# Kernel optimization log

Hardware: AMD Instinct MI355X
Metric: run time of the kernel (lower is better)

The kernel has to match this reference:

```python
import jax, jax.numpy as jnp
import numpy as np

EPS = 1e-12  # matches torch F.normalize default eps

def _l2_normalize(x):
    # torch.nn.functional.normalize: x / max(||x||_2, eps)
    n = jnp.sqrt(jnp.sum(x * x, axis=-1, keepdims=True))
    return x / jnp.maximum(n, EPS)

def setup_inputs() -> dict:
    key = jax.random.key(0)
    kq, kk, kv = jax.random.split(key, 3)
    B, N, M, C = 8, 4096, 4096, 256
    return {
        "query": jax.random.normal(kq, (B, N, C), dtype=jnp.float32),
        "key": jax.random.normal(kk, (B, M, C), dtype=jnp.float32),
        "value": jax.random.normal(kv, (B, M, C), dtype=jnp.float32),
    }

def reference(query, key, value):
    B, N, C = query.shape
    q = _l2_normalize(query)          # (B, N, C)
    k = _l2_normalize(key)            # (B, M, C)
    kv = jnp.einsum('bmc,bmd->bcd', k, value)   # (B, C, C)
    context = jnp.einsum('bnc,bcd->bnd', q, kv) # (B, N, C)
    return context / N
```

## Files before the change

### kernel.cpp

```cpp
#include <hip/hip_runtime.h>

typedef __attribute__((ext_vector_type(4))) float v4f;
typedef __attribute__((ext_vector_type(8))) short short8;
typedef unsigned short u16;
typedef __attribute__((ext_vector_type(4))) unsigned short u16x4;
typedef __attribute__((ext_vector_type(8))) unsigned short u16x8;

#define CDIM 256
#define NB 8
#define NN 4096
#define MM 4096

static __device__ __forceinline__ u16 f2bf(float f) {
  unsigned u = __float_as_uint(f);
  u = (u + 0x7fffu + ((u >> 16) & 1u)) >> 16;
  return (u16)u;
}
static __device__ __forceinline__ float bf2f(u16 h) {
  return __uint_as_float(((unsigned)h) << 16);
}

__global__ __launch_bounds__(256) void knorm_kernel(const float* __restrict__ key,
                                                    float* __restrict__ sk) {
  int t = threadIdx.x;
  int lane = t & 63;
  int r = blockIdx.x * 4 + (t >> 6);
  const v4f x = *(const v4f*)(key + (size_t)r * CDIM + lane * 4);
  float ss = x[0]*x[0] + x[1]*x[1] + x[2]*x[2] + x[3]*x[3];
  #pragma unroll
  for (int m = 1; m < 64; m <<= 1) ss += __shfl_xor(ss, m);
  if (lane == 0) sk[r] = 1.0f / fmaxf(sqrtf(ss), 1e-12f);
}

__global__ __launch_bounds__(512, 2) void kv_kernel(const float* __restrict__ key,
                                                    const float* __restrict__ value,
                                                    const float* __restrict__ sk,
                                                    u16* __restrict__ partial, int KC) {
  __shared__ __align__(16) u16 knT[256 * 64];
  __shared__ __align__(16) u16 vT[256 * 64];
  int t = threadIdx.x;
  int b = blockIdx.y, s = blockIdx.x;
  int w = t >> 6, lane = t & 63, lo = lane & 15, hi = lane >> 4;
  int cstage = t & 255, wq = t >> 8;

  v4f acc[2][16];
  #pragma unroll
  for (int i = 0; i < 2; i++)
    #pragma unroll
    for (int d = 0; d < 16; d++) acc[i][d] = (v4f){0.f, 0.f, 0.f, 0.f};

  int nsc = KC >> 6;
  for (int sc = 0; sc < nsc; ++sc) {
    int mbase = s * KC + sc * 64;
    #pragma unroll
    for (int it = 0; it < 8; ++it) {
      int ml0 = it * 8 + wq * 4;
      int gr = b * MM + mbase + ml0;
      size_t grow = (size_t)gr * CDIM + cstage;
      float k0 = key[grow], k1 = key[grow + CDIM], k2 = key[grow + 2 * CDIM], k3 = key[grow + 3 * CDIM];
      float s0 = sk[gr], s1 = sk[gr + 1], s2 = sk[gr + 2], s3 = sk[gr + 3];
      u16x4 kn = { f2bf(k0 * s0), f2bf(k1 * s1), f2bf(k2 * s2), f2bf(k3 * s3) };
      int idx = (cstage * 64 + ml0) ^ ((cstage & 7) << 3);
      *(u16x4*)&knT[idx] = kn;
      float v0 = value[grow], v1 = value[grow + CDIM], v2 = value[grow + 2 * CDIM], v3 = value[grow + 3 * CDIM];
      u16x4 vn = { f2bf(v0), f2bf(v1), f2bf(v2), f2bf(v3) };
      *(u16x4*)&vT[idx] = vn;
    }
    __syncthreads();
    #pragma unroll
    for (int kk = 0; kk < 64; kk += 32) {
      int acol = kk + hi * 8;
      int r0 = w * 32 + lo, r1 = w * 32 + 16 + lo;
      short8 a0 = *(const short8*)&knT[(r0 * 64 + acol) ^ ((r0 & 7) << 3)];
      short8 a1 = *(const short8*)&knT[(r1 * 64 + acol) ^ ((r1 & 7) << 3)];
      #pragma unroll
      for (int dt = 0; dt < 16; ++dt) {
        int drow = dt * 16 + lo;
        short8 bb = *(const short8*)&vT[(drow * 64 + acol) ^ ((drow & 7) << 3)];
        acc[0][dt] = __builtin_amdgcn_mfma_f32_16x16x32_bf16(bb, a0, acc[0][dt], 0, 0, 0);
        acc[1][dt] = __builtin_amdgcn_mfma_f32_16x16x32_bf16(bb, a1, acc[1][dt], 0, 0, 0);
      }
    }
    __syncthreads();
  }
  size_t base = ((size_t)(s * NB + b)) << 16;
  #pragma unroll
  for (int i = 0; i < 2; i++) {
    int cc = w * 32 + i * 16 + lo;
    #pragma unroll
    for (int dt = 0; dt < 16; ++dt) {
      int dd = dt * 16 + hi * 4;
      #pragma unroll
      for (int r = 0; r < 4; r++)
        partial[base + (size_t)(dd + r) * 256 + cc] = f2bf(acc[i][dt][r]);
    }
  }
}

__global__ __launch_bounds__(256) void red_kernel(const u16* __restrict__ partial,
                                                  u16* __restrict__ kvT, int splits) {
  int j = blockIdx.x * 256 + threadIdx.x;
  int b = j >> 13;
  int e0 = (j & 8191) * 8;
  size_t off = ((size_t)b << 16) + e0;
  const float inv = 1.0f / 4096.0f;
  float sum[8] = {0.f, 0.f, 0.f, 0.f, 0.f, 0.f, 0.f, 0.f};
  for (int s = 0; s < splits; ++s) {
    u16x8 p = *(const u16x8*)&partial[(((size_t)s * NB) << 16) + off];
    #pragma unroll
    for (int x = 0; x < 8; ++x) sum[x] += bf2f(p[x]);
  }
  u16x8 o;
  #pragma unroll
  for (int x = 0; x < 8; ++x) o[x] = f2bf(sum[x] * inv);
  *(u16x8*)&kvT[off] = o;
}

__global__ __launch_bounds__(512) void ctx_kernel(const float* __restrict__ query,
                                                  const u16* __restrict__ kvT,
                                                  float* __restrict__ out) {
  __shared__ __align__(16) u16 qn[16 * 256];
  int t = threadIdx.x;
  int b = blockIdx.y;
  int w = t >> 6, lane = t & 63, lo = lane & 15, hi = lane >> 4;
  const u16* kvb = kvT + ((size_t)b << 16);

  short8 Bf[2][8];
  #pragma unroll
  for (int i = 0; i < 2; i++) {
    int dr = (2 * w + i) * 16 + lo;
    #pragma unroll
    for (int kc = 0; kc < 8; kc++)
      Bf[i][kc] = *(const short8*)&kvb[(size_t)dr * 256 + kc * 32 + 8 * hi];
  }

  int row = t >> 5, l32 = t & 31;
  for (int nt = 0; nt < 4; ++nt) {
    int n0 = (blockIdx.x * 4 + nt) * 16;
    const float* qr = query + (size_t)(b * NN + n0 + row) * CDIM + l32 * 8;
    v4f x0 = *(const v4f*)qr;
    v4f x1 = *(const v4f*)(qr + 4);
    float ss = x0[0]*x0[0] + x0[1]*x0[1] + x0[2]*x0[2] + x0[3]*x0[3]
             + x1[0]*x1[0] + x1[1]*x1[1] + x1[2]*x1[2] + x1[3]*x1[3];
    #pragma unroll
    for (int m = 1; m < 32; m <<= 1) ss += __shfl_xor(ss, m);
    float sc = 1.0f / fmaxf(sqrtf(ss), 1e-12f);
    u16x8 qb;
    qb[0] = f2bf(x0[0] * sc); qb[1] = f2bf(x0[1] * sc);
    qb[2] = f2bf(x0[2] * sc); qb[3] = f2bf(x0[3] * sc);
    qb[4] = f2bf(x1[0] * sc); qb[5] = f2bf(x1[1] * sc);
    qb[6] = f2bf(x1[2] * sc); qb[7] = f2bf(x1[3] * sc);
    __syncthreads();
    *(u16x8*)&qn[(row * 256 + l32 * 8) ^ ((row & 7) << 3)] = qb;
    __syncthreads();
    short8 Af[8];
    #pragma unroll
    for (int kc = 0; kc < 8; kc++)
      Af[kc] = *(const short8*)&qn[(lo * 256 + kc * 32 + 8 * hi) ^ ((lo & 7) << 3)];
    v4f acc0 = (v4f){0.f, 0.f, 0.f, 0.f};
    v4f acc1 = (v4f){0.f, 0.f, 0.f, 0.f};
    #pragma unroll
    for (int kc = 0; kc < 8; kc++) {
      acc0 = __builtin_amdgcn_mfma_f32_16x16x32_bf16(Af[kc], Bf[0][kc], acc0, 0, 0, 0);
      acc1 = __builtin_amdgcn_mfma_f32_16x16x32_bf16(Af[kc], Bf[1][kc], acc1, 0, 0, 0);
    }
    #pragma unroll
    for (int r = 0; r < 4; r++) {
      size_t ro = (size_t)(b * NN + n0 + 4 * hi + r) * CDIM;
      out[ro + (2 * w) * 16 + lo] = acc0[r];
      out[ro + (2 * w + 1) * 16 + lo] = acc1[r];
    }
  }
}

extern "C" void kernel_launch(void* const* d_in, const int* in_sizes, int n_in,
                              void* d_out, int out_size, void* d_ws, size_t ws_size,
                              hipStream_t stream) {
  const float* q = (const float*)d_in[0];
  const float* k = (const float*)d_in[1];
  const float* v = (const float*)d_in[2];
  float* out = (float*)d_out;

  int splits = 32;
  while (splits > 2) {
    size_t need = 131072ull + ((size_t)splits + 1ull) * 1048576ull;
    if (need <= ws_size) break;
    splits >>= 1;
  }
  float* s_k = (float*)d_ws;
  u16* partial = (u16*)((char*)d_ws + 131072);
  u16* kvT = (u16*)((char*)d_ws + 131072 + (size_t)splits * 1048576ull);

  knorm_kernel<<<dim3(8192), dim3(256), 0, stream>>>(k, s_k);
  kv_kernel<<<dim3(splits, NB), dim3(512), 0, stream>>>(k, v, s_k, partial, MM / splits);
  red_kernel<<<dim3(256), dim3(256), 0, stream>>>(partial, kvT, splits);
  ctx_kernel<<<dim3(64, NB), dim3(512), 0, stream>>>(q, kvT, out);
}
```

Before: 66.46 us.

## Fuse key norm into kv kernel and spread ctx kernel over more blocks

Removes the separate key-normalization launch: each kv block now computes inverse norms for its own key rows into shared memory before the main loop, reading those rows from global memory an extra time but dropping a kernel launch and the global sk round-trip. The ctx kernel now handles one 16-row tile per block instead of four, with 4x more blocks, and issues the query load before the kvT fragment loads to overlap them. The cost is that each block reloads the kvT B-fragments, which adds L2 traffic.

Result: slower. 81.17 us (+22.1%).

```diff
diff --git a/kernel.cpp b/kernel.cpp
--- a/kernel.cpp
+++ b/kernel.cpp
@@ -20,28 +20,28 @@
   return __uint_as_float(((unsigned)h) << 16);
 }
 
-__global__ __launch_bounds__(256) void knorm_kernel(const float* __restrict__ key,
-                                                    float* __restrict__ sk) {
-  int t = threadIdx.x;
-  int lane = t & 63;
-  int r = blockIdx.x * 4 + (t >> 6);
-  const v4f x = *(const v4f*)(key + (size_t)r * CDIM + lane * 4);
-  float ss = x[0]*x[0] + x[1]*x[1] + x[2]*x[2] + x[3]*x[3];
-  #pragma unroll
-  for (int m = 1; m < 64; m <<= 1) ss += __shfl_xor(ss, m);
-  if (lane == 0) sk[r] = 1.0f / fmaxf(sqrtf(ss), 1e-12f);
-}
-
 __global__ __launch_bounds__(512, 2) void kv_kernel(const float* __restrict__ key,
                                                     const float* __restrict__ value,
-                                                    const float* __restrict__ sk,
                                                     u16* __restrict__ partial, int KC) {
   __shared__ __align__(16) u16 knT[256 * 64];
   __shared__ __align__(16) u16 vT[256 * 64];
+  __shared__ float skl[2048];
   int t = threadIdx.x;
   int b = blockIdx.y, s = blockIdx.x;
   int w = t >> 6, lane = t & 63, lo = lane & 15, hi = lane >> 4;
   int cstage = t & 255, wq = t >> 8;
+
+  int rpw = KC >> 3;
+  const float* kbase = key + (size_t)(b * MM + s * KC) * CDIM;
+  for (int i = 0; i < rpw; ++i) {
+    int m = w * rpw + i;
+    const v4f x = *(const v4f*)(kbase + (size_t)m * CDIM + lane * 4);
+    float ss = x[0]*x[0] + x[1]*x[1] + x[2]*x[2] + x[3]*x[3];
+    #pragma unroll
+    for (int mm = 1; mm < 64; mm <<= 1) ss += __shfl_xor(ss, mm);
+    if (lane == 0) skl[m] = 1.0f / fmaxf(sqrtf(ss), 1e-12f);
+  }
+  __syncthreads();
 
   v4f acc[2][16];
   #pragma unroll
@@ -56,9 +56,10 @@
     for (int it = 0; it < 8; ++it) {
       int ml0 = it * 8 + wq * 4;
       int gr = b * MM + mbase + ml0;
+      int lr = sc * 64 + ml0;
       size_t grow = (size_t)gr * CDIM + cstage;
       float k0 = key[grow], k1 = key[grow + CDIM], k2 = key[grow + 2 * CDIM], k3 = key[grow + 3 * CDIM];
-      float s0 = sk[gr], s1 = sk[gr + 1], s2 = sk[gr + 2], s3 = sk[gr + 3];
+      float s0 = skl[lr], s1 = skl[lr + 1], s2 = skl[lr + 2], s3 = skl[lr + 3];
       u16x4 kn = { f2bf(k0 * s0), f2bf(k1 * s1), f2bf(k2 * s2), f2bf(k3 * s3) };
       int idx = (cstage * 64 + ml0) ^ ((cstage & 7) << 3);
       *(u16x4*)&knT[idx] = kn;
@@ -122,9 +123,15 @@
   __shared__ __align__(16) u16 qn[16 * 256];
   int t = threadIdx.x;
   int b = blockIdx.y;
+  int n0 = blockIdx.x * 16;
   int w = t >> 6, lane = t & 63, lo = lane & 15, hi = lane >> 4;
+
+  int row = t >> 5, l32 = t & 31;
+  const float* qr = query + (size_t)(b * NN + n0 + row) * CDIM + l32 * 8;
+  v4f x0 = *(const v4f*)qr;
+  v4f x1 = *(const v4f*)(qr + 4);
+
   const u16* kvb = kvT + ((size_t)b << 16);
-
   short8 Bf[2][8];
   #pragma unroll
   for (int i = 0; i < 2; i++) {
@@ -134,42 +141,35 @@
       Bf[i][kc] = *(const short8*)&kvb[(size_t)dr * 256 + kc * 32 + 8 * hi];
   }
 
-  int row = t >> 5, l32 = t & 31;
-  for (int nt = 0; nt < 4; ++nt) {
-    int n0 = (blockIdx.x * 4 + nt) * 16;
-    const float* qr = query + (size_t)(b * NN + n0 + row) * CDIM + l32 * 8;
-    v4f x0 = *(const v4f*)qr;
-    v4f x1 = *(const v4f*)(qr + 4);
-    float ss = x0[0]*x0[0] + x0[1]*x0[1] + x0[2]*x0[2] + x0[3]*x0[3]
-             + x1[0]*x1[0] + x1[1]*x1[1] + x1[2]*x1[2] + x1[3]*x1[3];
-    #pragma unroll
-    for (int m = 1; m < 32; m <<= 1) ss += __shfl_xor(ss, m);
-    float sc = 1.0f / fmaxf(sqrtf(ss), 1e-12f);
-    u16x8 qb;
-    qb[0] = f2bf(x0[0] * sc); qb[1] = f2bf(x0[1] * sc);
-    qb[2] = f2bf(x0[2] * sc); qb[3] = f2bf(x0[3] * sc);
-    qb[4] = f2bf(x1[0] * sc); qb[5] = f2bf(x1[1] * sc);
-    qb[6] = f2bf(x1[2] * sc); qb[7] = f2bf(x1[3] * sc);
-    __syncthreads();
-    *(u16x8*)&qn[(row * 256 + l32 * 8) ^ ((row & 7) << 3)] = qb;
-    __syncthreads();
-    short8 Af[8];
-    #pragma unroll
-    for (int kc = 0; kc < 8; kc++)
-      Af[kc] = *(const short8*)&qn[(lo * 256 + kc * 32 + 8 * hi) ^ ((lo & 7) << 3)];
-    v4f acc0 = (v4f){0.f, 0.f, 0.f, 0.f};
-    v4f acc1 = (v4f){0.f, 0.f, 0.f, 0.f};
-    #pragma unroll
-    for (int kc = 0; kc < 8; kc++) {
-      acc0 = __builtin_amdgcn_mfma_f32_16x16x32_bf16(Af[kc], Bf[0][kc], acc0, 0, 0, 0);
-      acc1 = __builtin_amdgcn_mfma_f32_16x16x32_bf16(Af[kc], Bf[1][kc], acc1, 0, 0, 0);
-    }
-    #pragma unroll
-    for (int r = 0; r < 4; r++) {
-      size_t ro = (size_t)(b * NN + n0 + 4 * hi + r) * CDIM;
-      out[ro + (2 * w) * 16 + lo] = acc0[r];
-      out[ro + (2 * w + 1) * 16 + lo] = acc1[r];
-    }
+  float ss = x0[0]*x0[0] + x0[1]*x0[1] + x0[2]*x0[2] + x0[3]*x0[3]
+           + x1[0]*x1[0] + x1[1]*x1[1] + x1[2]*x1[2] + x1[3]*x1[3];
+  #pragma unroll
+  for (int m = 1; m < 32; m <<= 1) ss += __shfl_xor(ss, m);
+  float sc = 1.0f / fmaxf(sqrtf(ss), 1e-12f);
+  u16x8 qb;
+  qb[0] = f2bf(x0[0] * sc); qb[1] = f2bf(x0[1] * sc);
+  qb[2] = f2bf(x0[2] * sc); qb[3] = f2bf(x0[3] * sc);
+  qb[4] = f2bf(x1[0] * sc); qb[5] = f2bf(x1[1] * sc);
+  qb[6] = f2bf(x1[2] * sc); qb[7] = f2bf(x1[3] * sc);
+  *(u16x8*)&qn[(row * 256 + l32 * 8) ^ ((row & 7) << 3)] = qb;
+  __syncthreads();
+
+  short8 Af[8];
+  #pragma unroll
+  for (int kc = 0; kc < 8; kc++)
+    Af[kc] = *(const short8*)&qn[(lo * 256 + kc * 32 + 8 * hi) ^ ((lo & 7) << 3)];
+  v4f acc0 = (v4f){0.f, 0.f, 0.f, 0.f};
+  v4f acc1 = (v4f){0.f, 0.f, 0.f, 0.f};
+  #pragma unroll
+  for (int kc = 0; kc < 8; kc++) {
+    acc0 = __builtin_amdgcn_mfma_f32_16x16x32_bf16(Af[kc], Bf[0][kc], acc0, 0, 0, 0);
+    acc1 = __builtin_amdgcn_mfma_f32_16x16x32_bf16(Af[kc], Bf[1][kc], acc1, 0, 0, 0);
+  }
+  #pragma unroll
+  for (int r = 0; r < 4; r++) {
+    size_t ro = (size_t)(b * NN + n0 + 4 * hi + r) * CDIM;
+    out[ro + (2 * w) * 16 + lo] = acc0[r];
+    out[ro + (2 * w + 1) * 16 + lo] = acc1[r];
   }
 }
 
@@ -183,16 +183,14 @@
 
   int splits = 32;
   while (splits > 2) {
-    size_t need = 131072ull + ((size_t)splits + 1ull) * 1048576ull;
+    size_t need = ((size_t)splits + 1ull) * 1048576ull;
     if (need <= ws_size) break;
     splits >>= 1;
   }
-  float* s_k = (float*)d_ws;
-  u16* partial = (u16*)((char*)d_ws + 131072);
-  u16* kvT = (u16*)((char*)d_ws + 131072 + (size_t)splits * 1048576ull);
+  u16* partial = (u16*)d_ws;
+  u16* kvT = (u16*)((char*)d_ws + (size_t)splits * 1048576ull);
 
-  knorm_kernel<<<dim3(8192), dim3(256), 0, stream>>>(k, s_k);
-  kv_kernel<<<dim3(splits, NB), dim3(512), 0, stream>>>(k, v, s_k, partial, MM / splits);
+  kv_kernel<<<dim3(splits, NB), dim3(512), 0, stream>>>(k, v, partial, MM / splits);
   red_kernel<<<dim3(256), dim3(256), 0, stream>>>(partial, kvT, splits);
-  ctx_kernel<<<dim3(64, NB), dim3(512), 0, stream>>>(q, kvT, out);
+  ctx_kernel<<<dim3(256, NB), dim3(512), 0, stream>>>(q, kvT, out);
 }
```
